# Performance work log

Hardware: AMD Instinct MI355X
Metric: run time of the kernel (lower is better)

Reference implementation:

```python
import jax, jax.numpy as jnp
import numpy as np

N_NODES = 20000
N_EDGES = 160000
IN_SIZE = 128
HIDDEN = 256
N_HID_LAYERS = 2
OUT_SIZE = 32
N_GRAPHS = 16
NUM_MP = 4  # BASELINE_MESSAGE_PASSING (weights SHARED across rounds: [Sequential(...)]*N)
NEG_SLOPE = 0.01  # torch.nn.LeakyReLU default
W_SCALE = 0.05


def leaky(x):
    return jnp.where(x >= 0, x, NEG_SLOPE * x)


def wide_mlp(h, Win, bin_, Wh, bh, Wout, bout):
    # Linear(in,H) + act, then N_HID_LAYERS x (Linear(H,H) + act), then Linear(H,out)
    h = leaky(h @ Win + bin_)
    for l in range(Wh.shape[0]):  # small fixed layer count
        h = leaky(h @ Wh[l] + bh[l])
    return h @ Wout + bout


def setup_inputs() -> dict:
    key = jax.random.key(0)
    ks = jax.random.split(key, 16)
    d = {
        "x": jax.random.normal(ks[0], (N_NODES, IN_SIZE), jnp.float32),
        "edge_index": jax.random.randint(ks[1], (2, N_EDGES), 0, N_NODES, jnp.int64),
        "batch": jnp.sort(jax.random.randint(ks[2], (N_NODES,), 0, N_GRAPHS, jnp.int64)),
        "enc_Win": W_SCALE * jax.random.normal(ks[3], (IN_SIZE, HIDDEN), jnp.float32),
        "enc_bin": jnp.zeros((HIDDEN,), jnp.float32),
        "enc_Wh": W_SCALE * jax.random.normal(ks[4], (N_HID_LAYERS, HIDDEN, HIDDEN), jnp.float32),
        "enc_bh": jnp.zeros((N_HID_LAYERS, HIDDEN), jnp.float32),
        "enc_Wout": W_SCALE * jax.random.normal(ks[5], (HIDDEN, HIDDEN), jnp.float32),
        "enc_bout": jnp.zeros((HIDDEN,), jnp.float32),
        "edge_W": W_SCALE * jax.random.normal(ks[6], (3 * HIDDEN, HIDDEN), jnp.float32),
        "edge_b": jnp.zeros((HIDDEN,), jnp.float32),
        "proc_Win": W_SCALE * jax.random.normal(ks[7], (HIDDEN, HIDDEN), jnp.float32),
        "proc_bin": jnp.zeros((HIDDEN,), jnp.float32),
        "proc_Wh": W_SCALE * jax.random.normal(ks[8], (N_HID_LAYERS, HIDDEN, HIDDEN), jnp.float32),
        "proc_bh": jnp.zeros((N_HID_LAYERS, HIDDEN), jnp.float32),
        "proc_Wout": W_SCALE * jax.random.normal(ks[9], (HIDDEN, HIDDEN), jnp.float32),
        "proc_bout": jnp.zeros((HIDDEN,), jnp.float32),
        "dec_Win": W_SCALE * jax.random.normal(ks[10], (3 * HIDDEN, HIDDEN), jnp.float32),
        "dec_bin": jnp.zeros((HIDDEN,), jnp.float32),
        "dec_Wh": W_SCALE * jax.random.normal(ks[11], (N_HID_LAYERS, HIDDEN, HIDDEN), jnp.float32),
        "dec_bh": jnp.zeros((N_HID_LAYERS, HIDDEN), jnp.float32),
        "dec_Wout": W_SCALE * jax.random.normal(ks[12], (HIDDEN, OUT_SIZE), jnp.float32),
        "dec_bout": jnp.zeros((OUT_SIZE,), jnp.float32),
    }
    return d


def reference(x, edge_index, batch,
              enc_Win, enc_bin, enc_Wh, enc_bh, enc_Wout, enc_bout,
              edge_W, edge_b,
              proc_Win, proc_bin, proc_Wh, proc_bh, proc_Wout, proc_bout,
              dec_Win, dec_bin, dec_Wh, dec_bh, dec_Wout, dec_bout):
    n = x.shape[0]
    # encode
    h = wide_mlp(x, enc_Win, enc_bin, enc_Wh, enc_bh, enc_Wout, enc_bout)
    # add_self_loops
    loops = jnp.arange(n, dtype=edge_index.dtype)
    ei = jnp.concatenate([edge_index, jnp.stack([loops, loops])], axis=1)
    src, dst = ei[0], ei[1]  # PyG: j = ei[0] (source), i = ei[1] (target/aggregation index)
    e = jnp.zeros((ei.shape[1], HIDDEN), h.dtype)  # edge_attr None branch -> zeros
    # BASELINE_MESSAGE_PASSING rounds, shared weights
    for _ in range(NUM_MP):
        m = jnp.concatenate([h[dst], h[src], e], axis=-1) @ edge_W + edge_b  # [E+N, H]
        h = jax.ops.segment_sum(m, dst, num_segments=n)  # aggr='add'
        h = wide_mlp(h, proc_Win, proc_bin, proc_Wh, proc_bh, proc_Wout, proc_bout)
    # global mean / max / add pooling over graphs
    sums = jax.ops.segment_sum(h, batch, num_segments=N_GRAPHS)
    cnt = jax.ops.segment_sum(jnp.ones((n, 1), h.dtype), batch, num_segments=N_GRAPHS)
    mean = sums / jnp.maximum(cnt, 1.0)
    mx = jax.ops.segment_max(h, batch, num_segments=N_GRAPHS)
    pooled = jnp.concatenate([mean, mx, sums], axis=-1)  # [G, 3H]
    out = wide_mlp(pooled, dec_Win, dec_bin, dec_Wh, dec_bh, dec_Wout, dec_bout)
    return out
```

## Files before the change

### kernel.cpp

```cpp
#include <hip/hip_runtime.h>
#include <hip/hip_bf16.h>
#include <cstdint>

#define HID 256
#define NGRAPH 16
#define NEG_SLOPE 0.01f

typedef __bf16 bf16x8 __attribute__((ext_vector_type(8)));
typedef float f32x4 __attribute__((ext_vector_type(4)));

__device__ __forceinline__ float leaky(float x) { return x >= 0.f ? x : NEG_SLOPE * x; }

__device__ __forceinline__ ushort f2b(float f) {
  uint u = __float_as_uint(f);
  uint r = (u + 0x7fffu + ((u >> 16) & 1u)) >> 16;
  return (ushort)r;
}
__device__ __forceinline__ float b2f(ushort b) { return __uint_as_float((uint)b << 16); }

__global__ __launch_bounds__(256) void k_zero_i32(int* p, int n) {
  int i = blockIdx.x * blockDim.x + threadIdx.x;
  if (i < n) p[i] = 0;
}

__global__ __launch_bounds__(256) void k_hist(const int* __restrict__ key, int* __restrict__ cnt, int ne) {
  int e = blockIdx.x * blockDim.x + threadIdx.x;
  if (e < ne) atomicAdd(&cnt[key[e]], 1);
}

__global__ __launch_bounds__(1024) void k_scan(const int* __restrict__ cnt, int* __restrict__ rowptr,
                                               int* __restrict__ cursor, int n) {
  __shared__ int sd[1024];
  int tid = threadIdx.x;
  int CH = n / 1024 + 1;
  int base = tid * CH;
  int s = 0;
  for (int i = 0; i < CH; ++i) { int idx = base + i; if (idx < n) s += cnt[idx]; }
  sd[tid] = s;
  __syncthreads();
  for (int off = 1; off < 1024; off <<= 1) {
    int v = (tid >= off) ? sd[tid - off] : 0;
    __syncthreads();
    sd[tid] += v;
    __syncthreads();
  }
  int run = (tid == 0) ? 0 : sd[tid - 1];
  for (int i = 0; i < CH; ++i) {
    int idx = base + i;
    if (idx <= n) {
      rowptr[idx] = run;
      if (idx < n) { cursor[idx] = run; run += cnt[idx]; }
    }
  }
}

__global__ __launch_bounds__(64) void k_gbounds(const int* __restrict__ batch, int n,
                                                int* __restrict__ gstart, int* __restrict__ gcnt) {
  int t = threadIdx.x;
  if (t <= NGRAPH) {
    int lo = 0, hi = n;
    while (lo < hi) { int mid = (lo + hi) >> 1; if (batch[mid] < t) lo = mid + 1; else hi = mid; }
    gstart[t] = lo;
  }
  __syncthreads();
  if (t < NGRAPH) gcnt[t] = gstart[t + 1] - gstart[t];
}

__global__ __launch_bounds__(256) void k_scatter(const int* __restrict__ src, const int* __restrict__ dst,
                                                 int* __restrict__ cursor, int* __restrict__ col, int ne) {
  int e = blockIdx.x * blockDim.x + threadIdx.x;
  if (e < ne) {
    int d = dst[e];
    int pos = atomicAdd(&cursor[d], 1);
    col[pos] = src[e];
  }
}

__global__ __launch_bounds__(256) void k_f2b(const float* __restrict__ src, ushort* __restrict__ dst, int nElem) {
  int i = (blockIdx.x * 256 + threadIdx.x) * 4;
  if (i + 3 < nElem) {
    float4 v = *(const float4*)&src[i];
    ushort4 o;
    o.x = f2b(v.x); o.y = f2b(v.y); o.z = f2b(v.z); o.w = f2b(v.w);
    *(ushort4*)&dst[i] = o;
  } else {
    for (int j = i; j < nElem; ++j) dst[j] = f2b(src[j]);
  }
}

struct WconvArgs {
  const float* src[9];
  ushort* dst[9];
  int K[9];
};

__global__ __launch_bounds__(256) void k_wconv_all(WconvArgs args) {
  __shared__ float t[32][33];
  const int e = blockIdx.z;
  const int K = args.K[e];
  const int k0 = blockIdx.x * 32;
  if (k0 >= K) return;
  const float* src = args.src[e];
  ushort* dst = args.dst[e];
  const int n0 = blockIdx.y * 32;
  const int tx = threadIdx.x & 31;
  const int ty = threadIdx.x >> 5;
#pragma unroll
  for (int r = 0; r < 4; ++r) t[ty + 8 * r][tx] = src[(size_t)(k0 + ty + 8 * r) * 256 + n0 + tx];
  __syncthreads();
#pragma unroll
  for (int r = 0; r < 4; ++r) dst[(size_t)(n0 + ty + 8 * r) * K + k0 + tx] = f2b(t[tx][ty + 8 * r]);
}

__global__ __launch_bounds__(256) void k_aggregate(const ushort* __restrict__ h, const int* __restrict__ rowptr,
                                                   const int* __restrict__ col, ushort* __restrict__ S,
                                                   ushort* __restrict__ hd, float* __restrict__ degf, int n) {
  int node = blockIdx.x * 4 + (threadIdx.x >> 6);
  if (node >= n) return;
  int lane = threadIdx.x & 63;
  const ushort4* h4 = (const ushort4*)h;
  size_t base = (size_t)node * 64 + lane;
  ushort4 self = h4[base];
  float a0 = b2f(self.x), a1 = b2f(self.y), a2 = b2f(self.z), a3 = b2f(self.w);
  float s0 = a0, s1 = a1, s2 = a2, s3 = a3;
  int beg = rowptr[node], end = rowptr[node + 1];
  int p = beg;
  for (; p + 4 <= end; p += 4) {
    int j0 = col[p], j1 = col[p + 1], j2 = col[p + 2], j3 = col[p + 3];
    ushort4 v0 = h4[(size_t)j0 * 64 + lane];
    ushort4 v1 = h4[(size_t)j1 * 64 + lane];
    ushort4 v2 = h4[(size_t)j2 * 64 + lane];
    ushort4 v3 = h4[(size_t)j3 * 64 + lane];
    s0 += b2f(v0.x) + b2f(v1.x) + b2f(v2.x) + b2f(v3.x);
    s1 += b2f(v0.y) + b2f(v1.y) + b2f(v2.y) + b2f(v3.y);
    s2 += b2f(v0.z) + b2f(v1.z) + b2f(v2.z) + b2f(v3.z);
    s3 += b2f(v0.w) + b2f(v1.w) + b2f(v2.w) + b2f(v3.w);
  }
  for (; p < end; ++p) {
    int j = col[p];
    ushort4 v = h4[(size_t)j * 64 + lane];
    s0 += b2f(v.x); s1 += b2f(v.y); s2 += b2f(v.z); s3 += b2f(v.w);
  }
  float deg = (float)(end - beg + 1);
  ushort4 so; so.x = f2b(s0); so.y = f2b(s1); so.z = f2b(s2); so.w = f2b(s3);
  ((ushort4*)S)[base] = so;
  ushort4 ho; ho.x = f2b(deg * a0); ho.y = f2b(deg * a1); ho.z = f2b(deg * a2); ho.w = f2b(deg * a3);
  ((ushort4*)hd)[base] = ho;
  if (lane == 0) degf[node] = deg;
}

struct MLPArgs {
  const ushort* A0;
  const ushort* A1;
  const ushort* W0b;
  const ushort* W[5];
  const float* bias[5];
  const float* degf;
  ushort* out;
  int ldw0;
  int actf[5];
};

template <int NL, int K0, bool DUAL>
__global__ __launch_bounds__(256, 2) void k_mlp(MLPArgs args, int M) {
  constexpr int KS0 = K0 >> 5;
  constexpr int NT0 = (DUAL ? 2 : 1) * KS0;

  __shared__ ushort act[8 * 32 * 32];
  __shared__ __align__(16) ushort As[3][32 * 32];
  __shared__ __align__(16) ushort Bs[3][256 * 32];

  const int m0 = blockIdx.x * 32;
  const int tid = threadIdx.x;
  const int lane = tid & 63;
  const int wn = tid >> 6;
  const int rl = lane & 15;
  const int kg = lane >> 4;

  float biasv[NL][4];
#pragma unroll
  for (int L = 0; L < NL; ++L)
#pragma unroll
    for (int fn = 0; fn < 4; ++fn)
      biasv[L][fn] = args.bias[L][wn * 64 + fn * 16 + rl];
  float degv[8];
#pragma unroll
  for (int i = 0; i < 8; ++i) degv[i] = 1.0f;
  if (DUAL) {
#pragma unroll
    for (int fm = 0; fm < 2; ++fm)
#pragma unroll
      for (int rg = 0; rg < 4; ++rg)
        degv[fm * 4 + rg] = args.degf[m0 + fm * 16 + kg * 4 + rg];
  }
  __builtin_amdgcn_sched_barrier(0);
  asm volatile("s_waitcnt vmcnt(0)" ::: "memory");
  __builtin_amdgcn_sched_barrier(0);

  const int sa_slot = tid & 127;
  const int a_row = sa_slot >> 2;
  const int a_kg = (sa_slot & 3) ^ ((a_row >> 1) & 3);
  const int s_row = tid >> 2;
  const int s_sl = tid & 3;
  int ga = m0 + a_row; if (ga > M - 1) ga = M - 1;

  auto stageA = [&](int buf, const ushort* Ap, int k0s) {
    const ushort* src = Ap + (size_t)ga * K0 + k0s + a_kg * 8;
    __builtin_amdgcn_global_load_lds(
        (const __attribute__((address_space(1))) void*)src,
        (__attribute__((address_space(3))) void*)&As[buf][sa_slot * 8], 16, 0, 0);
  };
  auto stageB = [&](int buf, const ushort* Wp, int ldw, int k0s) {
#pragma unroll
    for (int i = 0; i < 4; ++i) {
      int row = s_row + 64 * i;
      int kgi = s_sl ^ ((row >> 1) & 3);
      const ushort* src = Wp + (size_t)row * ldw + k0s + kgi * 8;
      __builtin_amdgcn_global_load_lds(
          (const __attribute__((address_space(1))) void*)src,
          (__attribute__((address_space(3))) void*)&Bs[buf][(tid + 256 * i) * 8], 16, 0, 0);
    }
  };

  int rr_[2], sA_[2], rn_[4], sB_[4];
#pragma unroll
  for (int fm = 0; fm < 2; ++fm) {
    rr_[fm] = fm * 16 + rl;
    sA_[fm] = kg ^ ((rr_[fm] >> 1) & 3);
  }
#pragma unroll
  for (int fn = 0; fn < 4; ++fn) {
    rn_[fn] = wn * 64 + fn * 16 + rl;
    sB_[fn] = kg ^ ((rn_[fn] >> 1) & 3);
  }

  f32x4 acc[2][4];

  auto epilogue = [&](bool useDeg, int af_, bool toGlobal,
                      float bv0, float bv1, float bv2, float bv3) {
    float bvs[4] = {bv0, bv1, bv2, bv3};
#pragma unroll
    for (int fn = 0; fn < 4; ++fn) {
      int c = wn * 64 + fn * 16 + rl;
      float bv = bvs[fn];
      int ch = c >> 5, g = (c >> 3) & 3, e = c & 7;
#pragma unroll
      for (int fm = 0; fm < 2; ++fm) {
        int lrow0 = fm * 16 + kg * 4;
#pragma unroll
        for (int rg = 0; rg < 4; ++rg) {
          int lrow = lrow0 + rg;
          float rs = useDeg ? degv[fm * 4 + rg] : 1.0f;
          float v = acc[fm][fn][rg] + rs * bv;
          if (af_) v = leaky(v);
          if (toGlobal) {
            args.out[(size_t)(m0 + lrow) * 256 + c] = f2b(v);
          } else {
            int slot = g ^ ((lrow >> 1) & 3);
            act[ch * 1024 + lrow * 32 + slot * 8 + e] = f2b(v);
          }
        }
      }
    }
  };

#define WAITV(n)                                              \
  __builtin_amdgcn_sched_barrier(0);                          \
  asm volatile("s_waitcnt vmcnt(" #n ")" ::: "memory");       \
  __builtin_amdgcn_sched_barrier(0);

#pragma unroll
  for (int i = 0; i < 2; ++i)
#pragma unroll
    for (int j = 0; j < 4; ++j) acc[i][j] = (f32x4)(0.f);

  stageA(0, args.A0, 0);
  stageB(0, args.W[0], args.ldw0, 0);

#pragma unroll
  for (int t = 0; t < NT0; ++t) {
    if (t + 1 < NT0) {
      const int tp = t + 1;
      const int pass = DUAL ? (tp >= KS0 ? 1 : 0) : 0;
      const int k0s = (tp & (KS0 - 1)) << 5;
      stageA(tp % 3, pass ? args.A1 : args.A0, k0s);
      stageB(tp % 3, pass ? args.W0b : args.W[0], args.ldw0, k0s);
      WAITV(5)
    } else if (NL > 1) {
      stageB(NT0 % 3, args.W[1], 256, 0);
      WAITV(4)
    } else {
      WAITV(0)
    }
    __builtin_amdgcn_s_barrier();
    __builtin_amdgcn_sched_barrier(0);
    {
      const ushort* bA = &As[t % 3][0];
      const ushort* bB = &Bs[t % 3][0];
      bf16x8 afr[2], bfr[4];
#pragma unroll
      for (int fm = 0; fm < 2; ++fm) afr[fm] = *(const bf16x8*)&bA[rr_[fm] * 32 + sA_[fm] * 8];
#pragma unroll
      for (int fn = 0; fn < 4; ++fn) bfr[fn] = *(const bf16x8*)&bB[rn_[fn] * 32 + sB_[fn] * 8];
      __builtin_amdgcn_s_setprio(1);
#pragma unroll
      for (int fm = 0; fm < 2; ++fm)
#pragma unroll
        for (int fn = 0; fn < 4; ++fn)
          acc[fm][fn] = __builtin_amdgcn_mfma_f32_16x16x32_bf16(afr[fm], bfr[fn], acc[fm][fn], 0, 0, 0);
      __builtin_amdgcn_s_setprio(0);
    }
  }
  if (NL == 1) {
    epilogue(DUAL, args.actf[0], true, biasv[0][0], biasv[0][1], biasv[0][2], biasv[0][3]);
  } else {
    epilogue(DUAL, args.actf[0], false, biasv[0][0], biasv[0][1], biasv[0][2], biasv[0][3]);
    __syncthreads();
  }

#pragma unroll
  for (int L = 1; L < NL; ++L) {
    const int base = NT0 + 8 * (L - 1);
#pragma unroll
    for (int i = 0; i < 2; ++i)
#pragma unroll
      for (int j = 0; j < 4; ++j) acc[i][j] = (f32x4)(0.f);
#pragma unroll
    for (int t = 0; t < 8; ++t) {
      const int gs = base + t;
      if (t < 7) {
        stageB((gs + 1) % 3, args.W[L], 256, (t + 1) * 32);
        WAITV(4)
      } else if (L + 1 < NL) {
        stageB((gs + 1) % 3, args.W[L + 1], 256, 0);
        WAITV(4)
      } else {
        WAITV(0)
      }
      __builtin_amdgcn_s_barrier();
      __builtin_amdgcn_sched_barrier(0);
      {
        const ushort* bB = &Bs[gs % 3][0];
        bf16x8 afr[2], bfr[4];
#pragma unroll
        for (int fm = 0; fm < 2; ++fm)
          afr[fm] = *(const bf16x8*)&act[t * 1024 + rr_[fm] * 32 + sA_[fm] * 8];
#pragma unroll
        for (int fn = 0; fn < 4; ++fn) bfr[fn] = *(const bf16x8*)&bB[rn_[fn] * 32 + sB_[fn] * 8];
        __builtin_amdgcn_s_setprio(1);
#pragma unroll
        for (int fm = 0; fm < 2; ++fm)
#pragma unroll
          for (int fn = 0; fn < 4; ++fn)
            acc[fm][fn] = __builtin_amdgcn_mfma_f32_16x16x32_bf16(afr[fm], bfr[fn], acc[fm][fn], 0, 0, 0);
        __builtin_amdgcn_s_setprio(0);
      }
    }
    if (L == NL - 1) {
      epilogue(false, args.actf[L], true, biasv[L][0], biasv[L][1], biasv[L][2], biasv[L][3]);
    } else {
      __builtin_amdgcn_s_barrier();
      epilogue(false, args.actf[L], false, biasv[L][0], biasv[L][1], biasv[L][2], biasv[L][3]);
      __syncthreads();
    }
  }
#undef WAITV
}

__global__ __launch_bounds__(256) void k_dec_layer(
    const float* __restrict__ A, const float* __restrict__ W,
    const float* __restrict__ bias, float* __restrict__ out,
    int K, int N, int act)
{
  __shared__ float a[768];
  __shared__ float red[8][64];
  const int g = blockIdx.y;
  const int cols = (N >= 64) ? 64 : 32;
  const int segs = 256 / cols;
  const int t = threadIdx.x;
  const int col = t % cols, seg = t / cols;
  const int c = blockIdx.x * cols + col;
  for (int i = t; i < K; i += 256) a[i] = A[(size_t)g * K + i];
  __syncthreads();
  const int kper = K / segs;
  const int k0 = seg * kper;
  float p = 0.f;
#pragma unroll 8
  for (int k = k0; k < k0 + kper; ++k) p += a[k] * W[(size_t)k * N + c];
  red[seg][col] = p;
  __syncthreads();
  if (seg == 0) {
    float s = bias[c];
    for (int i = 0; i < segs; ++i) s += red[i][col];
    out[(size_t)g * N + c] = act ? leaky(s) : s;
  }
}

__global__ __launch_bounds__(256) void k_pool1(const ushort* __restrict__ h, const int* __restrict__ gstart,
                                               const int* __restrict__ gcnt, float* __restrict__ psum,
                                               float* __restrict__ pmax) {
  int g = blockIdx.x >> 4;
  int cch = blockIdx.x & 15;
  int t = threadIdx.x;
  int len = gcnt[g];
  int s0 = gstart[g];
  int chunk = (len + 15) >> 4;
  int i0 = s0 + cch * chunk;
  int i1 = min(i0 + chunk, s0 + len);
  float s = 0.f;
  float m = -3.402823466e+38f;
  for (int i = i0; i < i1; ++i) {
    float v = b2f(h[(size_t)i * HID + t]);
    s += v;
    m = fmaxf(m, v);
  }
  psum[(size_t)blockIdx.x * HID + t] = s;
  pmax[(size_t)blockIdx.x * HID + t] = m;
}

__global__ __launch_bounds__(256) void k_pool2(const float* __restrict__ psum, const float* __restrict__ pmax,
                                               const int* __restrict__ gcnt, float* __restrict__ pooled) {
  int g = blockIdx.x;
  int t = threadIdx.x;
  float s = 0.f, m = -3.402823466e+38f;
  for (int cch = 0; cch < 16; ++cch) {
    s += psum[(size_t)(g * 16 + cch) * HID + t];
    m = fmaxf(m, pmax[(size_t)(g * 16 + cch) * HID + t]);
  }
  float cf = (float)gcnt[g];
  pooled[g * 3 * HID + t] = s / fmaxf(cf, 1.f);
  pooled[g * 3 * HID + HID + t] = m;
  pooled[g * 3 * HID + 2 * HID + t] = s;
}

extern "C" void kernel_launch(void* const* d_in, const int* in_sizes, int n_in,
                              void* d_out, int out_size, void* d_ws, size_t ws_size,
                              hipStream_t stream) {
  const float* x        = (const float*)d_in[0];
  const int*   ei       = (const int*)d_in[1];
  const int*   batch    = (const int*)d_in[2];
  const float* enc_Win  = (const float*)d_in[3];
  const float* enc_bin  = (const float*)d_in[4];
  const float* enc_Wh   = (const float*)d_in[5];
  const float* enc_bh   = (const float*)d_in[6];
  const float* enc_Wout = (const float*)d_in[7];
  const float* enc_bout = (const float*)d_in[8];
  const float* edge_W   = (const float*)d_in[9];
  const float* edge_b   = (const float*)d_in[10];
  const float* proc_Win = (const float*)d_in[11];
  const float* proc_bin = (const float*)d_in[12];
  const float* proc_Wh  = (const float*)d_in[13];
  const float* proc_bh  = (const float*)d_in[14];
  const float* proc_Wout= (const float*)d_in[15];
  const float* proc_bout= (const float*)d_in[16];
  const float* dec_Win  = (const float*)d_in[17];
  const float* dec_bin  = (const float*)d_in[18];
  const float* dec_Wh   = (const float*)d_in[19];
  const float* dec_bh   = (const float*)d_in[20];
  const float* dec_Wout = (const float*)d_in[21];
  const float* dec_bout = (const float*)d_in[22];

  const int n  = in_sizes[0] / 128;
  const int ne = in_sizes[1] / 2;
  const int H = HID;

  char* p = (char*)d_ws;
  auto alloc = [&](size_t bytes) -> char* {
    char* r = p;
    p += (bytes + 255) & ~(size_t)255;
    return r;
  };
  ushort* hb1   = (ushort*)alloc((size_t)n * H * 2);
  ushort* Sb    = (ushort*)alloc((size_t)n * H * 2);
  ushort* hdb   = (ushort*)alloc((size_t)n * H * 2);
  ushort* xb    = (ushort*)alloc((size_t)n * 128 * 2);
  ushort* w_enc_in  = (ushort*)alloc((size_t)256 * 128 * 2);
  ushort* w_enc_h0  = (ushort*)alloc((size_t)256 * 256 * 2);
  ushort* w_enc_h1  = (ushort*)alloc((size_t)256 * 256 * 2);
  ushort* w_enc_out = (ushort*)alloc((size_t)256 * 256 * 2);
  ushort* w_proc_in  = (ushort*)alloc((size_t)256 * 256 * 2);
  ushort* w_proc_h0  = (ushort*)alloc((size_t)256 * 256 * 2);
  ushort* w_proc_h1  = (ushort*)alloc((size_t)256 * 256 * 2);
  ushort* w_proc_out = (ushort*)alloc((size_t)256 * 256 * 2);
  ushort* w_edge     = (ushort*)alloc((size_t)256 * 512 * 2);
  float* degf   = (float*)alloc((size_t)n * 4);
  float* pooled = (float*)alloc((size_t)NGRAPH * 3 * H * 4);
  float* psum   = (float*)alloc((size_t)256 * H * 4);
  float* pmax   = (float*)alloc((size_t)256 * H * 4);
  float* db0    = (float*)alloc((size_t)NGRAPH * H * 4);
  float* db1    = (float*)alloc((size_t)NGRAPH * H * 4);
  int* cnt    = (int*)alloc((size_t)n * 4);
  int* rowptr = (int*)alloc((size_t)(n + 1) * 4);
  int* cursor = (int*)alloc((size_t)n * 4);
  int* gstart = (int*)alloc((size_t)(NGRAPH + 1) * 4);
  int* gcnt   = (int*)alloc((size_t)NGRAPH * 4);
  int* colv   = (int*)alloc((size_t)ne * 4);

  const int* srcI = ei;
  const int* dstI = ei + ne;

  dim3 blk(256);

  WconvArgs wa;
  wa.src[0] = enc_Win;             wa.dst[0] = w_enc_in;   wa.K[0] = 128;
  wa.src[1] = enc_Wh;              wa.dst[1] = w_enc_h0;   wa.K[1] = 256;
  wa.src[2] = enc_Wh + 65536;      wa.dst[2] = w_enc_h1;   wa.K[2] = 256;
  wa.src[3] = enc_Wout;            wa.dst[3] = w_enc_out;  wa.K[3] = 256;
  wa.src[4] = proc_Win;            wa.dst[4] = w_proc_in;  wa.K[4] = 256;
  wa.src[5] = proc_Wh;             wa.dst[5] = w_proc_h0;  wa.K[5] = 256;
  wa.src[6] = proc_Wh + 65536;     wa.dst[6] = w_proc_h1;  wa.K[6] = 256;
  wa.src[7] = proc_Wout;           wa.dst[7] = w_proc_out; wa.K[7] = 256;
  wa.src[8] = edge_W;              wa.dst[8] = w_edge;     wa.K[8] = 512;
  k_wconv_all<<<dim3(16, 8, 9), blk, 0, stream>>>(wa);
  k_f2b<<<dim3((n * 128 / 4 + 255) / 256), blk, 0, stream>>>(x, xb, n * 128);

  k_zero_i32<<<dim3((n + 255) / 256), blk, 0, stream>>>(cnt, n);
  k_hist<<<dim3((ne + 255) / 256), blk, 0, stream>>>(dstI, cnt, ne);
  k_scan<<<1, 1024, 0, stream>>>(cnt, rowptr, cursor, n);
  k_gbounds<<<1, 64, 0, stream>>>(batch, n, gstart, gcnt);
  k_scatter<<<dim3((ne + 255) / 256), blk, 0, stream>>>(srcI, dstI, cursor, colv, ne);

  const int npanel = (n + 31) / 32;

  MLPArgs ea = {};
  ea.A0 = xb; ea.A1 = nullptr; ea.W0b = nullptr;
  ea.W[0] = w_enc_in; ea.W[1] = w_enc_h0; ea.W[2] = w_enc_h1; ea.W[3] = w_enc_out;
  ea.bias[0] = enc_bin; ea.bias[1] = enc_bh; ea.bias[2] = enc_bh + 256; ea.bias[3] = enc_bout;
  ea.bias[4] = enc_bout;
  ea.degf = nullptr; ea.out = hb1; ea.ldw0 = 128;
  ea.actf[0] = 1; ea.actf[1] = 1; ea.actf[2] = 1; ea.actf[3] = 0;
  k_mlp<4, 128, false><<<dim3(npanel), blk, 0, stream>>>(ea, n);

  MLPArgs pa = {};
  pa.A0 = hdb; pa.A1 = Sb; pa.W0b = w_edge + 256;
  pa.W[0] = w_edge; pa.W[1] = w_proc_in; pa.W[2] = w_proc_h0; pa.W[3] = w_proc_h1; pa.W[4] = w_proc_out;
  pa.bias[0] = edge_b; pa.bias[1] = proc_bin; pa.bias[2] = proc_bh; pa.bias[3] = proc_bh + 256; pa.bias[4] = proc_bout;
  pa.degf = degf; pa.out = hb1; pa.ldw0 = 512;
  pa.actf[0] = 0; pa.actf[1] = 1; pa.actf[2] = 1; pa.actf[3] = 1; pa.actf[4] = 0;

  for (int r = 0; r < 4; ++r) {
    k_aggregate<<<dim3((n + 3) / 4), blk, 0, stream>>>(hb1, rowptr, colv, Sb, hdb, degf, n);
    k_mlp<5, 256, true><<<dim3(npanel), blk, 0, stream>>>(pa, n);
  }

  k_pool1<<<dim3(NGRAPH * 16), blk, 0, stream>>>(hb1, gstart, gcnt, psum, pmax);
  k_pool2<<<dim3(NGRAPH), blk, 0, stream>>>(psum, pmax, gcnt, pooled);

  k_dec_layer<<<dim3(4, NGRAPH), blk, 0, stream>>>(pooled, dec_Win, dec_bin, db0, 768, 256, 1);
  k_dec_layer<<<dim3(4, NGRAPH), blk, 0, stream>>>(db0, dec_Wh, dec_bh, db1, 256, 256, 1);
  k_dec_layer<<<dim3(4, NGRAPH), blk, 0, stream>>>(db1, dec_Wh + 65536, dec_bh + 256, db0, 256, 256, 1);
  k_dec_layer<<<dim3(1, NGRAPH), blk, 0, stream>>>(db0, dec_Wout, dec_bout, (float*)d_out, 256, 32, 0);
}
```

Before: 398.4 us.

## Unify fused MLP k-steps into one loop with two-stage-ahead prefetch

Folds the first-layer loop and the hidden-layer loops of the fused MLP kernel into a single unrolled loop over all k-steps, prefetching two stages ahead into the triple buffer instead of one. Weight tiles for the next layer are now fetched before the current layer's epilogue, which is meant to hide global-to-LDS load latency better. The cost is an extra lgkmcnt wait plus a barrier after every step so a buffer is not overwritten while still being read, and deeper vmcnt accounting that has to match the number of loads issued per stage exactly.

```diff
diff --git a/kernel.cpp b/kernel.cpp
--- a/kernel.cpp
+++ b/kernel.cpp
@@ -165,6 +165,7 @@
 __global__ __launch_bounds__(256, 2) void k_mlp(MLPArgs args, int M) {
   constexpr int KS0 = K0 >> 5;
   constexpr int NT0 = (DUAL ? 2 : 1) * KS0;
+  constexpr int TOTAL = NT0 + 8 * (NL - 1);
 
   __shared__ ushort act[8 * 32 * 32];
   __shared__ __align__(16) ushort As[3][32 * 32];
@@ -221,6 +222,17 @@
           (__attribute__((address_space(3))) void*)&Bs[buf][(tid + 256 * i) * 8], 16, 0, 0);
     }
   };
+  auto stage_step = [&](int s) {
+    if (s < NT0) {
+      const int pass = DUAL ? (s >= KS0 ? 1 : 0) : 0;
+      const int k0s = (s & (KS0 - 1)) << 5;
+      stageA(s % 3, (DUAL && pass) ? args.A1 : args.A0, k0s);
+      stageB(s % 3, (DUAL && pass) ? args.W0b : args.W[0], args.ldw0, k0s);
+    } else {
+      const int q = s - NT0;
+      stageB(s % 3, args.W[1 + (q >> 3)], 256, (q & 7) << 5);
+    }
+  };
 
   int rr_[2], sA_[2], rn_[4], sB_[4];
 #pragma unroll
@@ -235,6 +247,10 @@
   }
 
   f32x4 acc[2][4];
+#pragma unroll
+  for (int i = 0; i < 2; ++i)
+#pragma unroll
+    for (int j = 0; j < 4; ++j) acc[i][j] = (f32x4)(0.f);
 
   auto epilogue = [&](bool useDeg, int af_, bool toGlobal,
                       float bv0, float bv1, float bv2, float bv3) {
@@ -264,42 +280,45 @@
     }
   };
 
-#define WAITV(n)                                              \
-  __builtin_amdgcn_sched_barrier(0);                          \
-  asm volatile("s_waitcnt vmcnt(" #n ")" ::: "memory");       \
-  __builtin_amdgcn_sched_barrier(0);
-
-#pragma unroll
-  for (int i = 0; i < 2; ++i)
-#pragma unroll
-    for (int j = 0; j < 4; ++j) acc[i][j] = (f32x4)(0.f);
-
-  stageA(0, args.A0, 0);
-  stageB(0, args.W[0], args.ldw0, 0);
-
-#pragma unroll
-  for (int t = 0; t < NT0; ++t) {
-    if (t + 1 < NT0) {
-      const int tp = t + 1;
-      const int pass = DUAL ? (tp >= KS0 ? 1 : 0) : 0;
-      const int k0s = (tp & (KS0 - 1)) << 5;
-      stageA(tp % 3, pass ? args.A1 : args.A0, k0s);
-      stageB(tp % 3, pass ? args.W0b : args.W[0], args.ldw0, k0s);
-      WAITV(5)
-    } else if (NL > 1) {
-      stageB(NT0 % 3, args.W[1], 256, 0);
-      WAITV(4)
-    } else {
-      WAITV(0)
+  auto waitv = [&](int w) {
+    __builtin_amdgcn_sched_barrier(0);
+    switch (w) {
+      case 0:  asm volatile("s_waitcnt vmcnt(0)"  ::: "memory"); break;
+      case 4:  asm volatile("s_waitcnt vmcnt(4)"  ::: "memory"); break;
+      case 5:  asm volatile("s_waitcnt vmcnt(5)"  ::: "memory"); break;
+      case 8:  asm volatile("s_waitcnt vmcnt(8)"  ::: "memory"); break;
+      case 9:  asm volatile("s_waitcnt vmcnt(9)"  ::: "memory"); break;
+      default: asm volatile("s_waitcnt vmcnt(10)" ::: "memory"); break;
+    }
+    __builtin_amdgcn_sched_barrier(0);
+  };
+
+  stage_step(0);
+  stage_step(1);
+
+#pragma unroll
+  for (int gs = 0; gs < TOTAL; ++gs) {
+    if (gs + 2 < TOTAL) stage_step(gs + 2);
+    {
+      const int l1 = (gs + 1 < TOTAL) ? ((gs + 1 < NT0) ? 5 : 4) : 0;
+      const int l2 = (gs + 2 < TOTAL) ? ((gs + 2 < NT0) ? 5 : 4) : 0;
+      waitv(l1 + l2);
     }
     __builtin_amdgcn_s_barrier();
     __builtin_amdgcn_sched_barrier(0);
     {
-      const ushort* bA = &As[t % 3][0];
-      const ushort* bB = &Bs[t % 3][0];
+      const ushort* bB = &Bs[gs % 3][0];
       bf16x8 afr[2], bfr[4];
-#pragma unroll
-      for (int fm = 0; fm < 2; ++fm) afr[fm] = *(const bf16x8*)&bA[rr_[fm] * 32 + sA_[fm] * 8];
+      if (gs < NT0) {
+        const ushort* bA = &As[gs % 3][0];
+#pragma unroll
+        for (int fm = 0; fm < 2; ++fm) afr[fm] = *(const bf16x8*)&bA[rr_[fm] * 32 + sA_[fm] * 8];
+      } else {
+        const int tloc = (gs - NT0) & 7;
+#pragma unroll
+        for (int fm = 0; fm < 2; ++fm)
+          afr[fm] = *(const bf16x8*)&act[tloc * 1024 + rr_[fm] * 32 + sA_[fm] * 8];
+      }
 #pragma unroll
       for (int fn = 0; fn < 4; ++fn) bfr[fn] = *(const bf16x8*)&bB[rn_[fn] * 32 + sB_[fn] * 8];
       __builtin_amdgcn_s_setprio(1);
@@ -310,61 +329,28 @@
           acc[fm][fn] = __builtin_amdgcn_mfma_f32_16x16x32_bf16(afr[fm], bfr[fn], acc[fm][fn], 0, 0, 0);
       __builtin_amdgcn_s_setprio(0);
     }
-  }
-  if (NL == 1) {
-    epilogue(DUAL, args.actf[0], true, biasv[0][0], biasv[0][1], biasv[0][2], biasv[0][3]);
-  } else {
-    epilogue(DUAL, args.actf[0], false, biasv[0][0], biasv[0][1], biasv[0][2], biasv[0][3]);
-    __syncthreads();
-  }
-
-#pragma unroll
-  for (int L = 1; L < NL; ++L) {
-    const int base = NT0 + 8 * (L - 1);
-#pragma unroll
-    for (int i = 0; i < 2; ++i)
-#pragma unroll
-      for (int j = 0; j < 4; ++j) acc[i][j] = (f32x4)(0.f);
-#pragma unroll
-    for (int t = 0; t < 8; ++t) {
-      const int gs = base + t;
-      if (t < 7) {
-        stageB((gs + 1) % 3, args.W[L], 256, (t + 1) * 32);
-        WAITV(4)
-      } else if (L + 1 < NL) {
-        stageB((gs + 1) % 3, args.W[L + 1], 256, 0);
-        WAITV(4)
+    __builtin_amdgcn_sched_barrier(0);
+    asm volatile("s_waitcnt lgkmcnt(0)" ::: "memory");
+    __builtin_amdgcn_sched_barrier(0);
+    __builtin_amdgcn_s_barrier();
+
+    const bool lend = (gs < NT0) ? (gs == NT0 - 1) : (((gs - NT0) & 7) == 7);
+    if (lend) {
+      const int Lc = (gs < NT0) ? 0 : 1 + ((gs - NT0) >> 3);
+      if (Lc == NL - 1) {
+        epilogue(DUAL && Lc == 0, args.actf[Lc], true,
+                 biasv[Lc][0], biasv[Lc][1], biasv[Lc][2], biasv[Lc][3]);
       } else {
-        WAITV(0)
+        epilogue(DUAL && Lc == 0, args.actf[Lc], false,
+                 biasv[Lc][0], biasv[Lc][1], biasv[Lc][2], biasv[Lc][3]);
+        __syncthreads();
+#pragma unroll
+        for (int i = 0; i < 2; ++i)
+#pragma unroll
+          for (int j = 0; j < 4; ++j) acc[i][j] = (f32x4)(0.f);
       }
-      __builtin_amdgcn_s_barrier();
-      __builtin_amdgcn_sched_barrier(0);
-      {
-        const ushort* bB = &Bs[gs % 3][0];
-        bf16x8 afr[2], bfr[4];
-#pragma unroll
-        for (int fm = 0; fm < 2; ++fm)
-          afr[fm] = *(const bf16x8*)&act[t * 1024 + rr_[fm] * 32 + sA_[fm] * 8];
-#pragma unroll
-        for (int fn = 0; fn < 4; ++fn) bfr[fn] = *(const bf16x8*)&bB[rn_[fn] * 32 + sB_[fn] * 8];
-        __builtin_amdgcn_s_setprio(1);
-#pragma unroll
-        for (int fm = 0; fm < 2; ++fm)
-#pragma unroll
-          for (int fn = 0; fn < 4; ++fn)
-            acc[fm][fn] = __builtin_amdgcn_mfma_f32_16x16x32_bf16(afr[fm], bfr[fn], acc[fm][fn], 0, 0, 0);
-        __builtin_amdgcn_s_setprio(0);
-      }
-    }
-    if (L == NL - 1) {
-      epilogue(false, args.actf[L], true, biasv[L][0], biasv[L][1], biasv[L][2], biasv[L][3]);
-    } else {
-      __builtin_amdgcn_s_barrier();
-      epilogue(false, args.actf[L], false, biasv[L][0], biasv[L][1], biasv[L][2], biasv[L][3]);
-      __syncthreads();
-    }
-  }
-#undef WAITV
+    }
+  }
 }
 
 __global__ __launch_bounds__(256) void k_dec_layer(
```

After: 490.3 us. +23.1%, slower.
